# Kernel optimization log

Measured on AMD Instinct MI355X. Metric: run time of the kernel, lower is better.

The kernel has to match this reference:

```python
import jax, jax.numpy as jnp
import numpy as np

HIDDEN = 2048
NUM_HEADS = 16
Q_LORA = 1536
KV_LORA = 512
QK_NOPE = 128
QK_ROPE = 64
V_HEAD = 128
EPS = 1e-6
QK_HEAD = QK_NOPE + QK_ROPE  # 192


def rmsnorm(x, w, eps=EPS):
    xf = x.astype(jnp.float32)
    var = jnp.mean(xf * xf, axis=-1, keepdims=True)
    return (w * (xf * jax.lax.rsqrt(var + eps)).astype(x.dtype))


def setup_inputs() -> dict:
    key = jax.random.key(0)
    ks = jax.random.split(key, 8)
    B, S = 1, 2048
    hidden_states = jax.random.normal(ks[0], (B, S, HIDDEN), dtype=jnp.float32)
    # causal additive mask [B,1,S,S]
    causal = jnp.tril(jnp.ones((S, S), dtype=bool))
    attention_mask = jnp.where(causal, 0.0, -1e9).astype(jnp.float32)[None, None]
    s = lambda fan_in: 1.0 / np.sqrt(fan_in)
    Wqa = jax.random.normal(ks[1], (HIDDEN, Q_LORA), dtype=jnp.float32) * s(HIDDEN)
    gqa = jnp.ones((Q_LORA,), dtype=jnp.float32)
    Wqb = jax.random.normal(ks[2], (Q_LORA, NUM_HEADS * QK_HEAD), dtype=jnp.float32) * s(Q_LORA)
    Wkva = jax.random.normal(ks[3], (HIDDEN, KV_LORA + QK_ROPE), dtype=jnp.float32) * s(HIDDEN)
    gkva = jnp.ones((KV_LORA,), dtype=jnp.float32)
    Wkvb = jax.random.normal(ks[4], (KV_LORA, NUM_HEADS * (QK_NOPE + V_HEAD)), dtype=jnp.float32) * s(KV_LORA)
    Wo = jax.random.normal(ks[5], (NUM_HEADS * V_HEAD, HIDDEN), dtype=jnp.float32) * s(NUM_HEADS * V_HEAD)
    return {"hidden_states": hidden_states, "attention_mask": attention_mask,
            "Wqa": Wqa, "gqa": gqa, "Wqb": Wqb, "Wkva": Wkva, "gkva": gkva,
            "Wkvb": Wkvb, "Wo": Wo}


def reference(hidden_states, attention_mask, Wqa, gqa, Wqb, Wkva, gkva, Wkvb, Wo):
    B, S, _ = hidden_states.shape
    # Q path: low-rank down-proj + RMSNorm + up-proj
    q_c = rmsnorm(hidden_states @ Wqa, gqa)
    q = (q_c @ Wqb).reshape(B, S, NUM_HEADS, QK_HEAD).transpose(0, 2, 1, 3)  # [B,H,S,192]
    # KV path: joint down-proj, split latent and shared rope part
    kv_c = hidden_states @ Wkva  # [B,S,KV_LORA+ROPE]
    kv_a, k_rope = kv_c[..., :KV_LORA], kv_c[..., KV_LORA:]
    kv = (rmsnorm(kv_a, gkva) @ Wkvb).reshape(B, S, NUM_HEADS, QK_NOPE + V_HEAD)
    k_nope, v = kv[..., :QK_NOPE], kv[..., QK_NOPE:]
    # shared rope part broadcast across heads (no rotary actually applied in source)
    k_rope_b = jnp.broadcast_to(k_rope[:, :, None, :], (B, S, NUM_HEADS, QK_ROPE))
    k = jnp.concatenate([k_nope, k_rope_b], axis=-1).transpose(0, 2, 1, 3)  # [B,H,S,192]
    v = v.transpose(0, 2, 1, 3)  # [B,H,S,128]
    scale = 1.0 / np.sqrt(QK_HEAD)
    attn = jnp.einsum("bhqd,bhkd->bhqk", q, k) * scale
    attn = attn + attention_mask
    attn = jax.nn.softmax(attn.astype(jnp.float32), axis=-1).astype(v.dtype)
    out = jnp.einsum("bhqk,bhkd->bhqd", attn, v)  # [B,H,S,128]
    out = out.transpose(0, 2, 1, 3).reshape(B, S, NUM_HEADS * V_HEAD)
    return out @ Wo
```

## Files before the change

kernel.cpp:

```cpp
#include <hip/hip_runtime.h>
#include <hip/hip_bf16.h>

typedef __bf16 bf16;
typedef __bf16 bf16x8 __attribute__((ext_vector_type(8)));
typedef __bf16 bf16x4 __attribute__((ext_vector_type(4)));
typedef float f32x4 __attribute__((ext_vector_type(4)));

#define HIDDEN 2048
#define SEQ 2048
#define NH 16
#define QL 1536
#define KVL 512
#define SCALE_LOG2E 0.10411754631f

__device__ __forceinline__ void gload_lds16(const void* g, void* l) {
  typedef const __attribute__((address_space(1))) void* gp_t;
  typedef __attribute__((address_space(3))) void* lp_t;
  __builtin_amdgcn_global_load_lds((gp_t)(unsigned long long)g,
                                   (lp_t)(unsigned int)(unsigned long long)l, 16, 0, 0);
}

__device__ __forceinline__ float fexp2(float x) {
  float r; asm("v_exp_f32 %0, %1" : "=v"(r) : "v"(x)); return r;
}
__device__ __forceinline__ unsigned cvt_pk_bf16(float lo, float hi) {
  unsigned r; asm("v_cvt_pk_bf16_f32 %0, %1, %2" : "=v"(r) : "v"(lo), "v"(hi)); return r;
}

__global__ void k_prep(const float* __restrict__ hidden, bf16* __restrict__ Xb,
                       const float* __restrict__ Wqa, bf16* __restrict__ WqaT,
                       const float* __restrict__ Wqb, bf16* __restrict__ WqbT,
                       const float* __restrict__ Wkva, bf16* __restrict__ WkvaT,
                       const float* __restrict__ Wkvb, bf16* __restrict__ WkvbT,
                       const float* __restrict__ Wo, bf16* __restrict__ WoT) {
  __shared__ float tile[32][33];
  int b = blockIdx.x, tid = threadIdx.x;
  const float* W; bf16* Wt; int K, N, bx, by;
  if (b < 3072)       { W = Wqa;  Wt = WqaT;  K = 2048; N = 1536; int r = b;         bx = r % 48;  by = r / 48; }
  else if (b < 7680)  { W = Wqb;  Wt = WqbT;  K = 1536; N = 3072; int r = b - 3072;  bx = r % 96;  by = r / 96; }
  else if (b < 8832)  { W = Wkva; Wt = WkvaT; K = 2048; N = 576;  int r = b - 7680;  bx = r % 18;  by = r / 18; }
  else if (b < 10880) { W = Wkvb; Wt = WkvbT; K = 512;  N = 4096; int r = b - 8832;  bx = r % 128; by = r / 128; }
  else if (b < 14976) { W = Wo;   Wt = WoT;   K = 2048; N = 2048; int r = b - 10880; bx = r % 64;  by = r / 64; }
  else {
    int r = b - 14976;
    int base = (r * 256 + tid) * 4;
    float4 v = *(const float4*)(hidden + base);
    bf16x4 o = { (bf16)v.x, (bf16)v.y, (bf16)v.z, (bf16)v.w };
    *(bf16x4*)(Xb + base) = o;
    return;
  }
  int n0 = bx * 32, k0 = by * 32, cc = tid & 31, rr = tid >> 5;
#pragma unroll
  for (int it = 0; it < 4; ++it) {
    int r = it * 8 + rr;
    tile[r][cc] = W[(size_t)(k0 + r) * N + n0 + cc];
  }
  __syncthreads();
#pragma unroll
  for (int it = 0; it < 4; ++it) {
    int r = it * 8 + rr;
    Wt[(size_t)(n0 + r) * K + k0 + cc] = (bf16)tile[cc][r];
  }
}

__device__ __forceinline__ void gemm_body(const bf16* __restrict__ A, const bf16* __restrict__ Bt,
                                          bf16* __restrict__ Cb, float* __restrict__ Cf,
                                          int N, int Kfull, int kbase, int Klen,
                                          int m0, int n0, bf16* As, bf16* Bs) {
  int tid = threadIdx.x, lane = tid & 63, w = tid >> 6;
  int wr = w >> 1, wc = w & 1;
  int l15 = lane & 15, l4 = lane >> 4;
  f32x4 acc[4][4] = {};
  for (int k0 = kbase; k0 < kbase + Klen; k0 += 64) {
#pragma unroll
    for (int i = 0; i < 4; ++i) {
      int c = w * 4 + i;
      int row = c * 8 + (lane >> 3);
      int col = (lane & 7) * 8;
      gload_lds16(&A[(size_t)(m0 + row) * Kfull + k0 + col], &As[c * 512]);
      gload_lds16(&Bt[(size_t)(n0 + row) * Kfull + k0 + col], &Bs[c * 512]);
    }
    __syncthreads();
#pragma unroll
    for (int kk = 0; kk < 2; ++kk) {
      bf16x8 af[4], bfr[4];
#pragma unroll
      for (int m = 0; m < 4; ++m)
        af[m] = *(const bf16x8*)&As[(wr * 64 + m * 16 + l15) * 64 + kk * 32 + l4 * 8];
#pragma unroll
      for (int n = 0; n < 4; ++n)
        bfr[n] = *(const bf16x8*)&Bs[(wc * 64 + n * 16 + l15) * 64 + kk * 32 + l4 * 8];
      __builtin_amdgcn_s_setprio(1);
#pragma unroll
      for (int m = 0; m < 4; ++m)
#pragma unroll
        for (int n = 0; n < 4; ++n)
          acc[m][n] = __builtin_amdgcn_mfma_f32_16x16x32_bf16(af[m], bfr[n], acc[m][n], 0, 0, 0);
      __builtin_amdgcn_s_setprio(0);
    }
    __syncthreads();
  }
#pragma unroll
  for (int m = 0; m < 4; ++m)
#pragma unroll
    for (int n = 0; n < 4; ++n)
#pragma unroll
      for (int r = 0; r < 4; ++r) {
        int grow = m0 + wr * 64 + m * 16 + l4 * 4 + r;
        int gcol = n0 + wc * 64 + n * 16 + l15;
        if (gcol < N) {
          float v = acc[m][n][r];
          if (Cf) Cf[(size_t)grow * N + gcol] = v;
          else Cb[(size_t)grow * N + gcol] = (bf16)v;
        }
      }
}

__global__ __launch_bounds__(256) void k_gemm_a(const bf16* __restrict__ Xb,
                                                const bf16* __restrict__ B1, const bf16* __restrict__ B2,
                                                float* __restrict__ qa0, float* __restrict__ qa1,
                                                float* __restrict__ kvc0, float* __restrict__ kvc1) {
  __shared__ __align__(16) bf16 As[128 * 64];
  __shared__ __align__(16) bf16 Bs[128 * 64];
  int by = blockIdx.y;
  if (by < 24) {
    int yy = by >> 1, kh = by & 1;
    gemm_body(Xb, B1, nullptr, kh ? qa1 : qa0, 1536, 2048, kh * 1024, 1024,
              blockIdx.x * 128, yy * 128, As, Bs);
  } else {
    int r = by - 24, yy = r >> 1, kh = r & 1;
    gemm_body(Xb, B2, nullptr, kh ? kvc1 : kvc0, 576, 2048, kh * 1024, 1024,
              blockIdx.x * 128, yy * 128, As, Bs);
  }
}

__global__ __launch_bounds__(256) void k_gemm_b(const bf16* __restrict__ A1, const bf16* __restrict__ A2,
                                                const bf16* __restrict__ B1, const bf16* __restrict__ B2,
                                                bf16* __restrict__ C1, bf16* __restrict__ C2) {
  __shared__ __align__(16) bf16 As[128 * 64];
  __shared__ __align__(16) bf16 Bs[128 * 64];
  int by = blockIdx.y;
  if (by < 24) gemm_body(A1, B1, C1, nullptr, 3072, 1536, 0, 1536, blockIdx.x * 128, by * 128, As, Bs);
  else         gemm_body(A2, B2, C2, nullptr, 4096, 512, 0, 512, blockIdx.x * 128, (by - 24) * 128, As, Bs);
}

__global__ __launch_bounds__(256) void k_gemm_sk(const bf16* __restrict__ A, const bf16* __restrict__ Bt,
                                                 float* __restrict__ O0, float* __restrict__ O1) {
  __shared__ __align__(16) bf16 As[128 * 64];
  __shared__ __align__(16) bf16 Bs[128 * 64];
  int by = blockIdx.y, nt = by >> 1, kh = by & 1;
  gemm_body(A, Bt, nullptr, kh ? O1 : O0, 2048, 2048, kh * 1024, 1024,
            blockIdx.x * 128, nt * 128, As, Bs);
}

__global__ void k_add(const float* __restrict__ O0, const float* __restrict__ O1,
                      float* __restrict__ out) {
  int base = (blockIdx.x * 256 + threadIdx.x) * 4;
  float4 a = *(const float4*)(O0 + base);
  float4 b = *(const float4*)(O1 + base);
  float4 o = { a.x + b.x, a.y + b.y, a.z + b.z, a.w + b.w };
  *(float4*)(out + base) = o;
}

__device__ inline float block_reduce_sum(float v, float* red) {
#pragma unroll
  for (int off = 1; off < 64; off <<= 1) v += __shfl_xor(v, off);
  int w = threadIdx.x >> 6;
  if ((threadIdx.x & 63) == 0) red[w] = v;
  __syncthreads();
  return red[0] + red[1] + red[2] + red[3];
}

__global__ void k_rms_all(const float* __restrict__ qa0, const float* __restrict__ qa1,
                          const float* __restrict__ gq, bf16* __restrict__ qc,
                          const float* __restrict__ kvc0, const float* __restrict__ kvc1,
                          const float* __restrict__ gkv,
                          bf16* __restrict__ kvn, bf16* __restrict__ kr) {
  __shared__ float red[4];
  int b = blockIdx.x, tid = threadIdx.x;
  if (b < 2048) {
    int row = b;
    float v[6];
    float ss = 0.f;
#pragma unroll
    for (int j = 0; j < 6; ++j) {
      size_t idx = (size_t)row * QL + tid + j * 256;
      v[j] = qa0[idx] + qa1[idx];
      ss += v[j] * v[j];
    }
    float tot = block_reduce_sum(ss, red);
    float rs = rsqrtf(tot / (float)QL + 1e-6f);
#pragma unroll
    for (int j = 0; j < 6; ++j) {
      int c = tid + j * 256;
      qc[(size_t)row * QL + c] = (bf16)(v[j] * rs * gq[c]);
    }
  } else {
    int row = b - 2048;
    size_t base = (size_t)row * 576;
    float v0 = kvc0[base + tid] + kvc1[base + tid];
    float v1 = kvc0[base + tid + 256] + kvc1[base + tid + 256];
    float tot = block_reduce_sum(v0 * v0 + v1 * v1, red);
    float rs = rsqrtf(tot / (float)KVL + 1e-6f);
    kvn[(size_t)row * KVL + tid] = (bf16)(v0 * rs * gkv[tid]);
    kvn[(size_t)row * KVL + tid + 256] = (bf16)(v1 * rs * gkv[tid + 256]);
    if (tid < 64) kr[row * 64 + tid] = (bf16)(kvc0[base + 512 + tid] + kvc1[base + 512 + tid]);
  }
}

__global__ void k_vt(const bf16* __restrict__ KVm, bf16* __restrict__ VT) {
  __shared__ bf16 tile[32][34];
  int b = blockIdx.x, tid = threadIdx.x;
  int h = b >> 8, rem = b & 255;
  int d0 = (rem >> 6) * 32, s0 = (rem & 63) * 32;
  int cc = tid & 31, rr = tid >> 5;
#pragma unroll
  for (int it = 0; it < 4; ++it) {
    int r = it * 8 + rr;
    tile[r][cc] = KVm[(size_t)(s0 + r) * 4096 + h * 256 + 128 + d0 + cc];
  }
  __syncthreads();
#pragma unroll
  for (int it = 0; it < 4; ++it) {
    int r = it * 8 + rr;
    VT[((size_t)(h * 128 + d0 + r)) * 2048 + s0 + cc] = tile[cc][r];
  }
}

__global__ __launch_bounds__(256) void k_attn(const bf16* __restrict__ Q, const bf16* __restrict__ KV,
                                              const bf16* __restrict__ KR, const bf16* __restrict__ VT,
                                              bf16* __restrict__ O) {
  __shared__ __align__(16) bf16 KsD[2][64 * 192];
  __shared__ __align__(16) bf16 VtD[2][128 * 64];
  int bid = blockIdx.x;
  int h = bid & 15, i = bid >> 4;
  int qb = (i < 16) ? i : 47 - i;
  int q0 = qb * 64;
  int tid = threadIdx.x, lane = tid & 63, w = tid >> 6;
  int l15 = lane & 15, l4 = lane >> 4;
  int sw = (l15 & 7) << 4;
  const bf16* VTh = VT + (size_t)h * 128 * 2048;

  bf16x8 aq[6];
  int qrow = q0 + w * 16 + l15;
#pragma unroll
  for (int ks = 0; ks < 6; ++ks)
    aq[ks] = *(const bf16x8*)&Q[(size_t)qrow * 3072 + h * 192 + ks * 32 + l4 * 8];

  f32x4 oacc[8] = {};
  float mrun = -1e30f, lrun = 0.f;
  int nt = qb + 1;

  auto STAGE = [&](int buf, int t) {
    char* kb = (char*)KsD[buf];
    char* vb = (char*)VtD[buf];
#pragma unroll
    for (int it = 0; it < 6; ++it) {
      int idx = it * 256 + tid;
      int r = idx / 24, gg = idx - r * 24;
      int c = gg ^ (r & 7);
      const bf16* src = (c < 16) ? &KV[(size_t)(t * 64 + r) * 4096 + h * 256 + c * 8]
                                 : &KR[(size_t)(t * 64 + r) * 64 + (c - 16) * 8];
      gload_lds16(src, kb + (it * 256 + w * 64) * 16);
    }
#pragma unroll
    for (int it = 0; it < 4; ++it) {
      int idx = it * 256 + tid;
      int d = idx >> 3, c2 = idx & 7, c = c2 ^ (d & 7);
      gload_lds16(&VTh[(size_t)d * 2048 + t * 64 + c * 8], vb + (it * 256 + w * 64) * 16);
    }
  };

  STAGE(0, 0);
  for (int t = 0; t < nt; ++t) {
    int cur = t & 1;
    if (t + 1 < nt) {
      STAGE(cur ^ 1, t + 1);
      asm volatile("s_waitcnt vmcnt(10)" ::: "memory");
    } else {
      asm volatile("s_waitcnt vmcnt(0)" ::: "memory");
    }
    __builtin_amdgcn_s_barrier();
    __builtin_amdgcn_sched_barrier(0);
    const char* Kb = (const char*)KsD[cur];
    const char* Vb = (const char*)VtD[cur];

    f32x4 sacc[4] = {};
    __builtin_amdgcn_s_setprio(1);
#pragma unroll
    for (int ks = 0; ks < 6; ++ks) {
      int co = (((ks << 2) + l4) << 4) ^ sw;
#pragma unroll
      for (int n = 0; n < 4; ++n) {
        bf16x8 ak = *(const bf16x8*)(Kb + (n * 16 + l15) * 384 + co);
        sacc[n] = __builtin_amdgcn_mfma_f32_16x16x32_bf16(ak, aq[ks], sacc[n], 0, 0, 0);
      }
    }
    __builtin_amdgcn_s_setprio(0);

    bool maskt = (t == qb);
#pragma unroll
    for (int n = 0; n < 4; ++n)
#pragma unroll
      for (int r = 0; r < 4; ++r) {
        float v = sacc[n][r] * SCALE_LOG2E;
        if (maskt) {
          int kvp = t * 64 + n * 16 + l4 * 4 + r;
          if (kvp > qrow) v = -1e30f;
        }
        sacc[n][r] = v;
      }

    float mx = sacc[0][0];
#pragma unroll
    for (int n = 0; n < 4; ++n)
#pragma unroll
      for (int r = 0; r < 4; ++r) mx = fmaxf(mx, sacc[n][r]);
    mx = fmaxf(mx, __shfl_xor(mx, 16));
    mx = fmaxf(mx, __shfl_xor(mx, 32));
    if (__any(mx - mrun > 8.0f)) {
      float mn = fmaxf(mrun, mx);
      float al = fexp2(mrun - mn);
      mrun = mn;
      lrun *= al;
#pragma unroll
      for (int vf = 0; vf < 8; ++vf) oacc[vf] *= al;
    }
    float rsum = 0.f;
    unsigned pk[4][2];
#pragma unroll
    for (int n = 0; n < 4; ++n) {
      float e0 = fexp2(sacc[n][0] - mrun);
      float e1 = fexp2(sacc[n][1] - mrun);
      float e2 = fexp2(sacc[n][2] - mrun);
      float e3 = fexp2(sacc[n][3] - mrun);
      rsum += (e0 + e1) + (e2 + e3);
      pk[n][0] = cvt_pk_bf16(e0, e1);
      pk[n][1] = cvt_pk_bf16(e2, e3);
    }
    rsum += __shfl_xor(rsum, 16);
    rsum += __shfl_xor(rsum, 32);
    lrun += rsum;

    int srcA = l15 + ((l4 & 1) << 5);
    int srcB = srcA + 16;
    int sel = l4 >> 1;
    __builtin_amdgcn_s_setprio(1);
#pragma unroll
    for (int ks = 0; ks < 2; ++ks) {
      unsigned a00 = (unsigned)__shfl((int)pk[2 * ks][0], srcA);
      unsigned a10 = (unsigned)__shfl((int)pk[2 * ks + 1][0], srcA);
      unsigned a01 = (unsigned)__shfl((int)pk[2 * ks][1], srcA);
      unsigned a11 = (unsigned)__shfl((int)pk[2 * ks + 1][1], srcA);
      unsigned b00 = (unsigned)__shfl((int)pk[2 * ks][0], srcB);
      unsigned b10 = (unsigned)__shfl((int)pk[2 * ks + 1][0], srcB);
      unsigned b01 = (unsigned)__shfl((int)pk[2 * ks][1], srcB);
      unsigned b11 = (unsigned)__shfl((int)pk[2 * ks + 1][1], srcB);
      union { unsigned u[4]; bf16x8 v; } ap;
      ap.u[0] = sel ? a10 : a00;
      ap.u[1] = sel ? a11 : a01;
      ap.u[2] = sel ? b10 : b00;
      ap.u[3] = sel ? b11 : b01;
      int co = (((ks << 2) + l4) << 4) ^ sw;
#pragma unroll
      for (int vf = 0; vf < 8; ++vf) {
        bf16x8 av = *(const bf16x8*)(Vb + (vf * 16 + l15) * 128 + co);
        oacc[vf] = __builtin_amdgcn_mfma_f32_16x16x32_bf16(av, ap.v, oacc[vf], 0, 0, 0);
      }
    }
    __builtin_amdgcn_s_setprio(0);
    __builtin_amdgcn_s_barrier();
  }

  int curF = (nt - 1) & 1;
  char* OTw = (char*)KsD[curF] + w * 4096;
  float inv = 1.0f / lrun;
#pragma unroll
  for (int vf = 0; vf < 8; ++vf) {
    unsigned ua = cvt_pk_bf16(oacc[vf][0] * inv, oacc[vf][1] * inv);
    unsigned ub = cvt_pk_bf16(oacc[vf][2] * inv, oacc[vf][3] * inv);
    int base = vf * 32 + l4 * 8;
    *(unsigned*)(OTw + l15 * 256 + ((base + 0) ^ sw)) = ua;
    *(unsigned*)(OTw + l15 * 256 + ((base + 4) ^ sw)) = ub;
  }
  int qq = lane >> 2, c0 = lane & 3;
  size_t obase = (size_t)(q0 + w * 16 + qq) * 2048 + h * 128;
#pragma unroll
  for (int ii = 0; ii < 4; ++ii) {
    int ck = ii * 4 + c0;
    bf16x8 v = *(const bf16x8*)(OTw + qq * 256 + ((ck * 16) ^ ((qq & 7) << 4)));
    *(bf16x8*)&O[obase + ck * 8] = v;
  }
}

extern "C" void kernel_launch(void* const* d_in, const int* in_sizes, int n_in,
                              void* d_out, int out_size, void* d_ws, size_t ws_size,
                              hipStream_t stream) {
  (void)in_sizes; (void)n_in; (void)out_size; (void)ws_size;
  const float* hidden = (const float*)d_in[0];
  const float* Wqa  = (const float*)d_in[2];
  const float* gqa  = (const float*)d_in[3];
  const float* Wqb  = (const float*)d_in[4];
  const float* Wkva = (const float*)d_in[5];
  const float* gkva = (const float*)d_in[6];
  const float* Wkvb = (const float*)d_in[7];
  const float* Wo   = (const float*)d_in[8];
  float* out = (float*)d_out;

  char* ws = (char*)d_ws;
  size_t off = 0;
  auto alloc = [&](size_t bytes) {
    char* p = ws + off;
    off += (bytes + 255) & ~(size_t)255;
    return p;
  };
  bf16* Xb     = (bf16*)alloc((size_t)SEQ * HIDDEN * 2);
  bf16* WqaT   = (bf16*)alloc((size_t)QL * HIDDEN * 2);
  bf16* WqbT   = (bf16*)alloc((size_t)3072 * QL * 2);
  bf16* WkvaT  = (bf16*)alloc((size_t)576 * HIDDEN * 2);
  bf16* WkvbT  = (bf16*)alloc((size_t)4096 * KVL * 2);
  bf16* WoT    = (bf16*)alloc((size_t)2048 * 2048 * 2);
  float* qa0   = (float*)alloc((size_t)SEQ * QL * 4);
  float* qa1   = (float*)alloc((size_t)SEQ * QL * 4);
  float* kvc0  = (float*)alloc((size_t)SEQ * 576 * 4);
  float* kvc1  = (float*)alloc((size_t)SEQ * 576 * 4);
  bf16* qc     = (bf16*)alloc((size_t)SEQ * QL * 2);
  bf16* kvn    = (bf16*)alloc((size_t)SEQ * KVL * 2);
  bf16* krope  = (bf16*)alloc((size_t)SEQ * 64 * 2);
  bf16* Qm     = (bf16*)alloc((size_t)SEQ * 3072 * 2);
  bf16* KVm    = (bf16*)alloc((size_t)SEQ * 4096 * 2);
  bf16* VTg    = (bf16*)alloc((size_t)NH * 128 * SEQ * 2);
  bf16* Om     = (bf16*)alloc((size_t)SEQ * 2048 * 2);
  float* O0 = qa0;
  float* O1 = (float*)KVm;

  k_prep<<<19072, 256, 0, stream>>>(hidden, Xb, Wqa, WqaT, Wqb, WqbT,
                                    Wkva, WkvaT, Wkvb, WkvbT, Wo, WoT);
  k_gemm_a<<<dim3(16, 34), 256, 0, stream>>>(Xb, WqaT, WkvaT, qa0, qa1, kvc0, kvc1);
  k_rms_all<<<4096, 256, 0, stream>>>(qa0, qa1, gqa, qc, kvc0, kvc1, gkva, kvn, krope);
  k_gemm_b<<<dim3(16, 56), 256, 0, stream>>>(qc, kvn, WqbT, WkvbT, Qm, KVm);
  k_vt<<<4096, 256, 0, stream>>>(KVm, VTg);
  k_attn<<<512, 256, 0, stream>>>(Qm, KVm, krope, VTg, Om);
  k_gemm_sk<<<dim3(16, 32), 256, 0, stream>>>(Om, WoT, O0, O1);
  k_add<<<4096, 256, 0, stream>>>(O0, O1, out);
}
```

Measured before the change: 219.7 us.

## Double-buffer LDS tiles in split-K GEMMs to overlap global loads with MFMA

Adds a prefetching GEMM body that stages the next K-tile into a second LDS buffer through direct global-to-LDS loads while MFMAs run on the current buffer. A partial vmcnt wait keeps only the current tile's loads outstanding. It is used in the down-projection GEMM and the output-projection split-K GEMM, with the epilogue factored into a shared helper. LDS use per block doubles to 64KB, which may reduce occupancy.

```diff
diff --git a/kernel.cpp b/kernel.cpp
--- a/kernel.cpp
+++ b/kernel.cpp
@@ -63,6 +63,27 @@
   }
 }
 
+__device__ __forceinline__ void gemm_epilogue(f32x4 acc[4][4], bf16* Cb, float* Cf,
+                                              int N, int m0, int n0) {
+  int lane = threadIdx.x & 63, w = threadIdx.x >> 6;
+  int wr = w >> 1, wc = w & 1;
+  int l15 = lane & 15, l4 = lane >> 4;
+#pragma unroll
+  for (int m = 0; m < 4; ++m)
+#pragma unroll
+    for (int n = 0; n < 4; ++n)
+#pragma unroll
+      for (int r = 0; r < 4; ++r) {
+        int grow = m0 + wr * 64 + m * 16 + l4 * 4 + r;
+        int gcol = n0 + wc * 64 + n * 16 + l15;
+        if (gcol < N) {
+          float v = acc[m][n][r];
+          if (Cf) Cf[(size_t)grow * N + gcol] = v;
+          else Cb[(size_t)grow * N + gcol] = (bf16)v;
+        }
+      }
+}
+
 __device__ __forceinline__ void gemm_body(const bf16* __restrict__ A, const bf16* __restrict__ Bt,
                                           bf16* __restrict__ Cb, float* __restrict__ Cf,
                                           int N, int Kfull, int kbase, int Klen,
@@ -100,37 +121,80 @@
     }
     __syncthreads();
   }
-#pragma unroll
-  for (int m = 0; m < 4; ++m)
-#pragma unroll
-    for (int n = 0; n < 4; ++n)
-#pragma unroll
-      for (int r = 0; r < 4; ++r) {
-        int grow = m0 + wr * 64 + m * 16 + l4 * 4 + r;
-        int gcol = n0 + wc * 64 + n * 16 + l15;
-        if (gcol < N) {
-          float v = acc[m][n][r];
-          if (Cf) Cf[(size_t)grow * N + gcol] = v;
-          else Cb[(size_t)grow * N + gcol] = (bf16)v;
-        }
-      }
+  gemm_epilogue(acc, Cb, Cf, N, m0, n0);
+}
+
+__device__ __forceinline__ void gemm_body_pf(const bf16* __restrict__ A, const bf16* __restrict__ Bt,
+                                             bf16* __restrict__ Cb, float* __restrict__ Cf,
+                                             int N, int Kfull, int kbase, int Klen,
+                                             int m0, int n0, bf16* AsD, bf16* BsD) {
+  int tid = threadIdx.x, lane = tid & 63, w = tid >> 6;
+  int wr = w >> 1, wc = w & 1;
+  int l15 = lane & 15, l4 = lane >> 4;
+  f32x4 acc[4][4] = {};
+
+  auto STAGE = [&](int buf, int k0) {
+#pragma unroll
+    for (int i = 0; i < 4; ++i) {
+      int c = w * 4 + i;
+      int row = c * 8 + (lane >> 3);
+      int col = (lane & 7) * 8;
+      gload_lds16(&A[(size_t)(m0 + row) * Kfull + k0 + col], &AsD[buf * 8192 + c * 512]);
+      gload_lds16(&Bt[(size_t)(n0 + row) * Kfull + k0 + col], &BsD[buf * 8192 + c * 512]);
+    }
+  };
+
+  int nT = Klen >> 6;
+  STAGE(0, kbase);
+  for (int tt = 0; tt < nT; ++tt) {
+    int cur = tt & 1;
+    if (tt + 1 < nT) {
+      STAGE(cur ^ 1, kbase + (tt + 1) * 64);
+      asm volatile("s_waitcnt vmcnt(8)" ::: "memory");
+    } else {
+      asm volatile("s_waitcnt vmcnt(0)" ::: "memory");
+    }
+    __builtin_amdgcn_s_barrier();
+    __builtin_amdgcn_sched_barrier(0);
+    const bf16* As = &AsD[cur * 8192];
+    const bf16* Bs = &BsD[cur * 8192];
+#pragma unroll
+    for (int kk = 0; kk < 2; ++kk) {
+      bf16x8 af[4], bfr[4];
+#pragma unroll
+      for (int m = 0; m < 4; ++m)
+        af[m] = *(const bf16x8*)&As[(wr * 64 + m * 16 + l15) * 64 + kk * 32 + l4 * 8];
+#pragma unroll
+      for (int n = 0; n < 4; ++n)
+        bfr[n] = *(const bf16x8*)&Bs[(wc * 64 + n * 16 + l15) * 64 + kk * 32 + l4 * 8];
+      __builtin_amdgcn_s_setprio(1);
+#pragma unroll
+      for (int m = 0; m < 4; ++m)
+#pragma unroll
+        for (int n = 0; n < 4; ++n)
+          acc[m][n] = __builtin_amdgcn_mfma_f32_16x16x32_bf16(af[m], bfr[n], acc[m][n], 0, 0, 0);
+      __builtin_amdgcn_s_setprio(0);
+    }
+    __builtin_amdgcn_s_barrier();
+  }
+  gemm_epilogue(acc, Cb, Cf, N, m0, n0);
 }
 
 __global__ __launch_bounds__(256) void k_gemm_a(const bf16* __restrict__ Xb,
                                                 const bf16* __restrict__ B1, const bf16* __restrict__ B2,
                                                 float* __restrict__ qa0, float* __restrict__ qa1,
                                                 float* __restrict__ kvc0, float* __restrict__ kvc1) {
-  __shared__ __align__(16) bf16 As[128 * 64];
-  __shared__ __align__(16) bf16 Bs[128 * 64];
+  __shared__ __align__(16) bf16 AsD[2 * 128 * 64];
+  __shared__ __align__(16) bf16 BsD[2 * 128 * 64];
   int by = blockIdx.y;
   if (by < 24) {
     int yy = by >> 1, kh = by & 1;
-    gemm_body(Xb, B1, nullptr, kh ? qa1 : qa0, 1536, 2048, kh * 1024, 1024,
-              blockIdx.x * 128, yy * 128, As, Bs);
+    gemm_body_pf(Xb, B1, nullptr, kh ? qa1 : qa0, 1536, 2048, kh * 1024, 1024,
+                 blockIdx.x * 128, yy * 128, AsD, BsD);
   } else {
     int r = by - 24, yy = r >> 1, kh = r & 1;
-    gemm_body(Xb, B2, nullptr, kh ? kvc1 : kvc0, 576, 2048, kh * 1024, 1024,
-              blockIdx.x * 128, yy * 128, As, Bs);
+    gemm_body_pf(Xb, B2, nullptr, kh ? kvc1 : kvc0, 576, 2048, kh * 1024, 1024,
+                 blockIdx.x * 128, yy * 128, AsD, BsD);
   }
 }
 
@@ -146,11 +210,11 @@
 
 __global__ __launch_bounds__(256) void k_gemm_sk(const bf16* __restrict__ A, const bf16* __restrict__ Bt,
                                                  float* __restrict__ O0, float* __restrict__ O1) {
-  __shared__ __align__(16) bf16 As[128 * 64];
-  __shared__ __align__(16) bf16 Bs[128 * 64];
+  __shared__ __align__(16) bf16 AsD[2 * 128 * 64];
+  __shared__ __align__(16) bf16 BsD[2 * 128 * 64];
   int by = blockIdx.y, nt = by >> 1, kh = by & 1;
-  gemm_body(A, Bt, nullptr, kh ? O1 : O0, 2048, 2048, kh * 1024, 1024,
-            blockIdx.x * 128, nt * 128, As, Bs);
+  gemm_body_pf(A, Bt, nullptr, kh ? O1 : O0, 2048, 2048, kh * 1024, 1024,
+               blockIdx.x * 128, nt * 128, AsD, BsD);
 }
 
 __global__ void k_add(const float* __restrict__ O0, const float* __restrict__ O1,
```

Result: faster. 204.2 us (median of 3 runs) (-7.0%).
